# Kernel optimization log

Measured on AMD Instinct MI355X. Metric: run time of the kernel, lower is better.

Reference implementation:

```python
import jax, jax.numpy as jnp
import numpy as np

L, H, M, KB = 8, 512, 32, 256  # layers, hidden, fourier modes, key bits
EPS = 1e-5


def setup_inputs() -> dict:
    key = jax.random.key(0)
    ks = jax.random.split(key, 20)
    B, S = 8, 2048
    s = 0.02
    return {
        'x': jax.random.normal(ks[0], (B, S), jnp.float32),
        # input projection Linear(1, H): weight [H] (squeezed), bias [H]
        'in_w': jax.random.normal(ks[1], (H,), jnp.float32) * s,
        'in_b': jax.random.normal(ks[2], (H,), jnp.float32) * s,
        # per-layer fourier weights (complex, stored as real/imag), conv1d(k=1), layernorm
        'fw_r': jax.random.normal(ks[3], (L, M, H, H), jnp.float32) * s,
        'fw_i': jax.random.normal(ks[4], (L, M, H, H), jnp.float32) * s,
        'conv_w': jax.random.normal(ks[5], (L, H, H), jnp.float32) / np.sqrt(H),
        'conv_b': jax.random.normal(ks[6], (L, H), jnp.float32) * s,
        'ln_g': jnp.ones((L, H), jnp.float32),
        'ln_b': jnp.zeros((L, H), jnp.float32),
        # output projection H -> H/2 -> H/4 -> 1
        'op1_w': jax.random.normal(ks[7], (H // 2, H), jnp.float32) / np.sqrt(H),
        'op1_b': jnp.zeros((H // 2,), jnp.float32),
        'op2_w': jax.random.normal(ks[8], (H // 4, H // 2), jnp.float32) / np.sqrt(H // 2),
        'op2_b': jnp.zeros((H // 4,), jnp.float32),
        'op3_w': jax.random.normal(ks[9], (1, H // 4), jnp.float32) / np.sqrt(H // 4),
        'op3_b': jnp.zeros((1,), jnp.float32),
        # cryptanalytic head H -> H -> KB (sigmoid)
        'h1_w': jax.random.normal(ks[10], (H, H), jnp.float32) / np.sqrt(H),
        'h1_b': jnp.zeros((H,), jnp.float32),
        'h2_w': jax.random.normal(ks[11], (KB, H), jnp.float32) / np.sqrt(H),
        'h2_b': jnp.zeros((KB,), jnp.float32),
    }


def _gelu(x):
    return jax.nn.gelu(x, approximate=False)


def _fourier_layer(x, Wc, cw, cb, g, b):
    # x: [B, S, H]; Wc: [M, H, H] complex
    S = x.shape[1]
    x_ft = jnp.fft.rfft(x, axis=1)  # [B, F, H] complex, F = S//2+1
    m = min(M, x_ft.shape[1])
    # batched per-mode complex GEMM (replaces python loop over modes)
    spec = jnp.einsum('bmh,mhk->bmk', x_ft[:, :m], Wc[:m])
    out_ft = jnp.concatenate([spec, jnp.zeros_like(x_ft[:, m:])], axis=1)
    x_fourier = jnp.fft.irfft(out_ft, n=S, axis=1)  # real [B, S, H]
    x_conv = x @ cw.T + cb  # Conv1d kernel-size-1 == per-position linear
    y = x_fourier + x_conv
    mu = jnp.mean(y, axis=-1, keepdims=True)
    var = jnp.var(y, axis=-1, keepdims=True)
    return (y - mu) * jax.lax.rsqrt(var + EPS) * g + b


def reference(x, in_w, in_b, fw_r, fw_i, conv_w, conv_b, ln_g, ln_b,
              op1_w, op1_b, op2_w, op2_b, op3_w, op3_b,
              h1_w, h1_b, h2_w, h2_b):
    # input projection: Linear(1, H) on x[..., None]
    h = x[:, :, None] * in_w[None, None, :] + in_b  # [B, S, H]
    Wc = fw_r + 1j * fw_i  # [L, M, H, H]
    for l in range(L):
        h = _fourier_layer(h, Wc[l], conv_w[l], conv_b[l], ln_g[l], ln_b[l]) + h
    # output projection (dropout is identity in eval)
    o = _gelu(h @ op1_w.T + op1_b)
    o = _gelu(o @ op2_w.T + op2_b)
    output = (o @ op3_w.T + op3_b)[..., 0]  # [B, S]
    gf = jnp.mean(h, axis=1)  # [B, H]
    k = _gelu(gf @ h1_w.T + h1_b)
    key_pred = jax.nn.sigmoid(k @ h2_w.T + h2_b)  # [B, KB]
    return output, key_pred
```

## Files before the change

kernel.cpp:

```cpp
#include <hip/hip_runtime.h>
#include <hip/hip_bf16.h>
#include <math.h>

#define BB   8
#define SEQ  2048
#define HD   512
#define LAY  8
#define MD   32
#define NKB  256
#define LNEPS 1e-5f

typedef __attribute__((ext_vector_type(8))) short v8s;
typedef __attribute__((ext_vector_type(4))) float v4f;
typedef __attribute__((ext_vector_type(4))) unsigned short v4us;

__device__ __forceinline__ float b2f(__hip_bfloat16 v) { return __bfloat162float(v); }
__device__ __forceinline__ float geluf(float v) { return v * 0.5f * (1.f + erff(v * 0.70710678118654752f)); }
__device__ __forceinline__ float bflo(unsigned int u) { return __uint_as_float((u & 0xFFFFu) << 16); }
__device__ __forceinline__ float bfhi(unsigned int u) { return __uint_as_float(u & 0xFFFF0000u); }

__device__ __forceinline__ float ldin(const void* p, size_t i, int bf) {
    if (bf) return __bfloat162float(((const __hip_bfloat16*)p)[i]);
    return ((const float*)p)[i];
}
__device__ __forceinline__ void stout(void* p, size_t i, float v, int bf) {
    if (bf) ((__hip_bfloat16*)p)[i] = __float2bfloat16(v);
    else    ((float*)p)[i] = v;
}

__device__ __forceinline__ void gl2lds16(const void* g, void* l) {
    __builtin_amdgcn_global_load_lds((__attribute__((address_space(1))) void*)g,
                                     (__attribute__((address_space(3))) void*)l, 16, 0, 0);
}

__global__ void k_flag(const unsigned int* __restrict__ lng_bits, int* __restrict__ flag) {
    if (threadIdx.x == 0 && blockIdx.x == 0)
        *flag = (lng_bits[0] == 0x3F803F80u) ? 1 : 0;
}

__global__ void k_setup(const void* __restrict__ x, const void* __restrict__ in_w, const void* __restrict__ in_b,
                        const void* __restrict__ cw, const void* __restrict__ w1, const void* __restrict__ w2,
                        const void* __restrict__ h1w, const void* __restrict__ h2w,
                        __hip_bfloat16* __restrict__ Ffwd, __hip_bfloat16* __restrict__ T2,
                        __hip_bfloat16* __restrict__ cwbf, __hip_bfloat16* __restrict__ w1bf,
                        __hip_bfloat16* __restrict__ w2bf, float* __restrict__ h1T, float* __restrict__ h2T,
                        float* __restrict__ h, __hip_bfloat16* __restrict__ hbf,
                        float* __restrict__ gf,
                        const int* __restrict__ flag) {
    int bf = *flag;
    int blk = blockIdx.x, t = threadIdx.x;
    if (blk < 512) {
        int idx = blk * 256 + t;
        int j = idx >> 11, s = idx & 2047;
        int m = j >> 1;
        int phase = (m * s) & (SEQ - 1);
        float ang = (float)phase * (6.283185307179586f / (float)SEQ);
        Ffwd[idx] = __float2bfloat16((j & 1) ? -sinf(ang) : cosf(ang));
    } else if (blk < 1024) {
        int idx = (blk - 512) * 256 + t;
        int s = idx >> 6, j = idx & 63;
        int m = j >> 1;
        float v;
        if (j == 0)      v = 1.f / (float)SEQ;
        else if (j == 1) v = 0.f;
        else {
            int phase = (m * s) & (SEQ - 1);
            float ang = (float)phase * (6.283185307179586f / (float)SEQ);
            v = (j & 1) ? (-2.f / (float)SEQ) * sinf(ang) : (2.f / (float)SEQ) * cosf(ang);
        }
        T2[idx] = __float2bfloat16(v);
    } else if (blk < 9216) {
        int idx = (blk - 1024) * 256 + t;
        cwbf[idx] = __float2bfloat16(ldin(cw, idx, bf));
    } else if (blk < 9728) {
        int idx = (blk - 9216) * 256 + t;
        w1bf[idx] = __float2bfloat16(ldin(w1, idx, bf));
    } else if (blk < 9856) {
        int idx = (blk - 9728) * 256 + t;
        w2bf[idx] = __float2bfloat16(ldin(w2, idx, bf));
    } else if (blk < 10880) {
        int idx = (blk - 9856) * 256 + t;
        int r = idx & 511, c = idx >> 9;
        h1T[idx] = ldin(h1w, (size_t)r * 512 + c, bf);
    } else if (blk < 11392) {
        int idx = (blk - 10880) * 256 + t;
        int r = idx & 255, c = idx >> 8;
        h2T[idx] = ldin(h2w, (size_t)r * 512 + c, bf);
    } else if (blk < 11408) {
        int idx = (blk - 11392) * 256 + t;
        gf[idx] = 0.f;
    } else {
        int idx = (blk - 11408) * 256 + t;
        int j = idx & 511;
        int bs = idx >> 9;
        float v = ldin(x, bs, bf) * ldin(in_w, j, bf) + ldin(in_b, j, bf);
        h[idx] = v;
        hbf[idx] = __float2bfloat16(v);
    }
}

__global__ __launch_bounds__(256) void k_fdft2(const __hip_bfloat16* __restrict__ hbf,
                                               const __hip_bfloat16* __restrict__ Ffwd,
                                               float* __restrict__ Xpart) {
    __shared__ __align__(16) __hip_bfloat16 Als[2][16 * 72];
    int t = threadIdx.x;
    int lane = t & 63, wv = t >> 6;
    int ln15 = lane & 15, quad = lane >> 4;
    int ht = blockIdx.x, b = blockIdx.y, kh = blockIdx.z;
    int kcs = kh * 16;
    int sr = t >> 2, hc = (t & 3) * 4;

    v4f acc = (v4f){0.f, 0.f, 0.f, 0.f};

    const __hip_bfloat16* asrc0 = hbf + (size_t)b * SEQ * HD + ht * 16;
    const __hip_bfloat16* fbase = Ffwd + (size_t)(wv * 16 + ln15) * SEQ + quad * 8;

    v4us cur = *(const v4us*)(asrc0 + (size_t)(kcs * 64 + sr) * HD + hc);
#pragma unroll
    for (int e = 0; e < 4; e++)
        Als[0][(hc + e) * 72 + sr] = ((const __hip_bfloat16*)&cur)[e];
    __syncthreads();
    for (int i = 0; i < 16; i++) {
        int buf = i & 1;
        v4us nxt = cur;
        if (i < 15)
            nxt = *(const v4us*)(asrc0 + (size_t)((kcs + i + 1) * 64 + sr) * HD + hc);
        v8s bf0 = *(const v8s*)(fbase + (kcs + i) * 64);
        v8s bf1 = *(const v8s*)(fbase + (kcs + i) * 64 + 32);
        v8s af0 = *(const v8s*)&Als[buf][ln15 * 72 + quad * 8];
        v8s af1 = *(const v8s*)&Als[buf][ln15 * 72 + 32 + quad * 8];
        acc = __builtin_amdgcn_mfma_f32_16x16x32_bf16(af0, bf0, acc, 0, 0, 0);
        acc = __builtin_amdgcn_mfma_f32_16x16x32_bf16(af1, bf1, acc, 0, 0, 0);
        if (i < 15) {
#pragma unroll
            for (int e = 0; e < 4; e++)
                Als[buf ^ 1][(hc + e) * 72 + sr] = ((const __hip_bfloat16*)&nxt)[e];
        }
        __syncthreads();
        cur = nxt;
    }
    int j = wv * 16 + ln15;
    int m = j >> 1, c = j & 1;
    int hg = ht * 16 + quad * 4;
    float* outp = Xpart + (size_t)kh * 262144 + (size_t)(b * 32 + m) * 1024;
#pragma unroll
    for (int r = 0; r < 4; r++)
        outp[(size_t)(hg + r) * 2 + c] = acc[r];
}

__global__ __launch_bounds__(512) void k_mix(const float* __restrict__ Xp0, const float* __restrict__ Xp1,
                                             const void* __restrict__ fwr, const void* __restrict__ fwi,
                                             __hip_bfloat16* __restrict__ spec2, int l,
                                             const int* __restrict__ flag) {
    int bf = *flag;
    int kt = blockIdx.x;
    int m  = blockIdx.y;
    int t = threadIdx.x;
    int kl = t & 15, hg = t >> 4;
    int k0 = kt * 64 + kl * 4;
    __shared__ float xs[8192];
    __shared__ float red[32 * 512];
    for (int e = t; e < 8192; e += 512) {
        int bb = e >> 10, r = e & 1023;
        size_t off = (size_t)(bb * 32 + m) * 1024 + r;
        xs[bb * 1024 + r] = Xp0[off] + Xp1[off];
    }
    __syncthreads();
    float ar[8][4], ai[8][4];
#pragma unroll
    for (int bb = 0; bb < 8; bb++)
#pragma unroll
        for (int q = 0; q < 4; q++) { ar[bb][q] = 0.f; ai[bb][q] = 0.f; }
    size_t wbase = (size_t)(l * 32 + m) * 262144 + k0;
    const float2* xs2 = (const float2*)xs;
    if (bf) {
        const __hip_bfloat16* fr = (const __hip_bfloat16*)fwr;
        const __hip_bfloat16* fi = (const __hip_bfloat16*)fwi;
#pragma unroll 2
        for (int hh = hg; hh < 512; hh += 32) {
            v4us urv = *(const v4us*)(fr + wbase + (size_t)hh * 512);
            v4us uiv = *(const v4us*)(fi + wbase + (size_t)hh * 512);
            float wr[4], wi[4];
#pragma unroll
            for (int q = 0; q < 4; q++) {
                wr[q] = __uint_as_float(((unsigned int)(unsigned short)urv[q]) << 16);
                wi[q] = __uint_as_float(((unsigned int)(unsigned short)uiv[q]) << 16);
            }
#pragma unroll
            for (int bb = 0; bb < 8; bb++) {
                float2 x2 = xs2[bb * 512 + hh];
#pragma unroll
                for (int q = 0; q < 4; q++) {
                    ar[bb][q] += x2.x * wr[q] - x2.y * wi[q];
                    ai[bb][q] += x2.x * wi[q] + x2.y * wr[q];
                }
            }
        }
    } else {
        const float* fr = (const float*)fwr;
        const float* fi = (const float*)fwi;
#pragma unroll 2
        for (int hh = hg; hh < 512; hh += 32) {
            v4f wrv = *(const v4f*)(fr + wbase + (size_t)hh * 512);
            v4f wiv = *(const v4f*)(fi + wbase + (size_t)hh * 512);
#pragma unroll
            for (int bb = 0; bb < 8; bb++) {
                float2 x2 = xs2[bb * 512 + hh];
#pragma unroll
                for (int q = 0; q < 4; q++) {
                    ar[bb][q] += x2.x * wrv[q] - x2.y * wiv[q];
                    ai[bb][q] += x2.x * wiv[q] + x2.y * wrv[q];
                }
            }
        }
    }
    v4f* red4 = (v4f*)red;
#pragma unroll
    for (int bb = 0; bb < 8; bb++)
        red4[hg * 128 + bb * 16 + kl] = (v4f){ar[bb][0], ar[bb][1], ar[bb][2], ar[bb][3]};
    __syncthreads();
    float sr = 0.f;
#pragma unroll
    for (int g = 0; g < 32; g++) sr += red[g * 512 + t];
    __syncthreads();
#pragma unroll
    for (int bb = 0; bb < 8; bb++)
        red4[hg * 128 + bb * 16 + kl] = (v4f){ai[bb][0], ai[bb][1], ai[bb][2], ai[bb][3]};
    __syncthreads();
    float si = 0.f;
#pragma unroll
    for (int g = 0; g < 32; g++) si += red[g * 512 + t];

    int bb = t >> 6, j = t & 63;
    int k = kt * 64 + j;
    size_t o = ((size_t)(bb * 512 + k) << 6) + 2 * m;
    __hip_bfloat16 hr = __float2bfloat16(sr), hi = __float2bfloat16(si);
    unsigned int pk = (unsigned int)*(unsigned short*)&hr | ((unsigned int)*(unsigned short*)&hi << 16);
    *(unsigned int*)(spec2 + o) = pk;
}

__global__ __launch_bounds__(512) void k_gln(__hip_bfloat16* __restrict__ hbf,
                                             const __hip_bfloat16* __restrict__ cwbf,
                                             const __hip_bfloat16* __restrict__ T2,
                                             const __hip_bfloat16* __restrict__ spec2,
                                             const void* __restrict__ cb,
                                             const void* __restrict__ lng, const void* __restrict__ lnb,
                                             float* __restrict__ h,
                                             int l, const int* __restrict__ flag) {
    int bfv = *flag;
    __shared__ __align__(16) __hip_bfloat16 smem[2][18432];
    __shared__ float stats[128];
    __hip_bfloat16* Yls = &smem[0][0];

    int t = threadIdx.x;
    int lane = t & 63, wv = t >> 6;
    int wr = wv >> 2, wc = wv & 3;
    int ln15 = lane & 15, quad = lane >> 4;
    int row0 = blockIdx.x * 64;
    int b = row0 >> 11, s0 = row0 & 2047;

    v4f acc[16];
#pragma unroll
    for (int i = 0; i < 16; i++) acc[i] = (v4f){0.f, 0.f, 0.f, 0.f};

    const __hip_bfloat16* cwl = cwbf + (size_t)l * 262144;

    auto stage = [&](int buf, int kc) {
        int k0 = kc * 32;
        if (t < 256) {
            int row = t >> 2, kq = (t & 3) * 8;
            const __hip_bfloat16* asrc = (k0 < 512)
                ? hbf + (size_t)(row0 + row) * 512 + k0 + kq
                : T2 + (size_t)(s0 + row) * 64 + (k0 - 512) + kq;
            gl2lds16(asrc, &smem[buf][(size_t)(wv * 64) * 8]);
        }
#pragma unroll
        for (int p = 0; p < 4; p++) {
            int i = p * 512 + t;
            int n = i >> 2, kq = (i & 3) * 8;
            const __hip_bfloat16* bsrc = (k0 < 512)
                ? cwl + (size_t)n * 512 + k0 + kq
                : spec2 + (size_t)(b * 512 + n) * 64 + (k0 - 512) + kq;
            gl2lds16(bsrc, &smem[buf][2048 + (size_t)(p * 512 + wv * 64) * 8]);
        }
    };

    stage(0, 0);
    __syncthreads();
    int cur = 0;
    for (int kc = 0; kc < 18; kc++) {
        if (kc < 17) stage(cur ^ 1, kc + 1);
        const __hip_bfloat16* Als = &smem[cur][0];
        const __hip_bfloat16* Bls = &smem[cur][2048];
        v8s af[2], bfr[8];
#pragma unroll
        for (int i = 0; i < 2; i++)
            af[i] = *(const v8s*)&Als[(wr * 32 + i * 16 + ln15) * 32 + quad * 8];
#pragma unroll
        for (int j = 0; j < 8; j++)
            bfr[j] = *(const v8s*)&Bls[(wc * 128 + j * 16 + ln15) * 32 + quad * 8];
#pragma unroll
        for (int i = 0; i < 2; i++)
#pragma unroll
            for (int j = 0; j < 8; j++)
                acc[i * 8 + j] = __builtin_amdgcn_mfma_f32_16x16x32_bf16(af[i], bfr[j], acc[i * 8 + j], 0, 0, 0);
        __syncthreads();
        cur ^= 1;
    }
#pragma unroll
    for (int j = 0; j < 8; j++) {
        int col = wc * 128 + j * 16 + ln15;
        float cbv = ldin(cb, l * HD + col, bfv);
#pragma unroll
        for (int i = 0; i < 2; i++) {
            int rl = wr * 32 + i * 16 + quad * 4;
#pragma unroll
            for (int r = 0; r < 4; r++)
                Yls[(rl + r) * 520 + col] = __float2bfloat16(acc[i * 8 + j][r] + cbv);
        }
    }
    __syncthreads();
    {
        int r = t >> 3, g = t & 7;
        float s = 0.f, q = 0.f;
        for (int i = 0; i < 32; i++) {
            int cp = g + i * 8;
            unsigned int u = *(const unsigned int*)&Yls[r * 520 + cp * 2];
            float v0 = bflo(u), v1 = bfhi(u);
            s += v0 + v1; q += v0 * v0 + v1 * v1;
        }
        s += __shfl_xor(s, 1); s += __shfl_xor(s, 2); s += __shfl_xor(s, 4);
        q += __shfl_xor(q, 1); q += __shfl_xor(q, 2); q += __shfl_xor(q, 4);
        if (g == 0) {
            float mu = s * (1.f / (float)HD);
            float var = q * (1.f / (float)HD) - mu * mu;
            stats[r * 2] = mu; stats[r * 2 + 1] = rsqrtf(var + LNEPS);
        }
    }
    __syncthreads();
    {
        int c2 = t & 255;
        int gc = 2 * c2;
        float g0 = ldin(lng, l * HD + gc, bfv),     g1 = ldin(lng, l * HD + gc + 1, bfv);
        float b0 = ldin(lnb, l * HD + gc, bfv),     b1 = ldin(lnb, l * HD + gc + 1, bfv);
        int rbase = t >> 8;
        for (int k = 0; k < 32; k++) {
            int r = rbase + 2 * k;
            float mu = stats[r * 2], rs = stats[r * 2 + 1];
            unsigned int u = *(const unsigned int*)&Yls[r * 520 + c2 * 2];
            float v0 = bflo(u), v1 = bfhi(u);
            float2 hv = *(const float2*)&h[(size_t)(row0 + r) * HD + gc];
            float n0 = (v0 - mu) * rs * g0 + b0 + hv.x;
            float n1 = (v1 - mu) * rs * g1 + b1 + hv.y;
            *(float2*)&h[(size_t)(row0 + r) * HD + gc] = (float2){n0, n1};
            __hip_bfloat16 a0 = __float2bfloat16(n0), a1 = __float2bfloat16(n1);
            unsigned int up = ((unsigned int)(*(unsigned short*)&a1) << 16) | (unsigned int)(*(unsigned short*)&a0);
            ((unsigned int*)(hbf + (size_t)(row0 + r) * HD))[c2] = up;
        }
    }
}

__global__ __launch_bounds__(256) void k_pj1(const __hip_bfloat16* __restrict__ hbf,
                                             const __hip_bfloat16* __restrict__ w1bf,
                                             const void* __restrict__ b1,
                                             __hip_bfloat16* __restrict__ o1bf,
                                             const int* __restrict__ flag) {
    int bfv = *flag;
    __shared__ __align__(16) __hip_bfloat16 smem[2][8192];
    int t = threadIdx.x;
    int lane = t & 63, wv = t >> 6;
    int wr = wv >> 1, wc = wv & 1;
    int ln15 = lane & 15, quad = lane >> 4;
    int row0 = blockIdx.x * 128, n0 = blockIdx.y * 128;

    v4f acc[16];
#pragma unroll
    for (int i = 0; i < 16; i++) acc[i] = (v4f){0.f, 0.f, 0.f, 0.f};

    auto stage = [&](int buf, int kc) {
        int k0 = kc * 32;
#pragma unroll
        for (int p = 0; p < 2; p++) {
            int i = p * 256 + t;
            int row = i >> 2, kq = (i & 3) * 8;
            gl2lds16(hbf + (size_t)(row0 + row) * 512 + k0 + kq, &smem[buf][(size_t)(p * 256 + wv * 64) * 8]);
            gl2lds16(w1bf + (size_t)(n0 + row) * 512 + k0 + kq, &smem[buf][4096 + (size_t)(p * 256 + wv * 64) * 8]);
        }
    };

    stage(0, 0);
    __syncthreads();
    int cur = 0;
    for (int kc = 0; kc < 16; kc++) {
        if (kc < 15) stage(cur ^ 1, kc + 1);
        const __hip_bfloat16* Als = &smem[cur][0];
        const __hip_bfloat16* Bls = &smem[cur][4096];
        v8s af[4], bfr[4];
#pragma unroll
        for (int i = 0; i < 4; i++)
            af[i] = *(const v8s*)&Als[(wr * 64 + i * 16 + ln15) * 32 + quad * 8];
#pragma unroll
        for (int j = 0; j < 4; j++)
            bfr[j] = *(const v8s*)&Bls[(wc * 64 + j * 16 + ln15) * 32 + quad * 8];
#pragma unroll
        for (int i = 0; i < 4; i++)
#pragma unroll
            for (int j = 0; j < 4; j++)
                acc[i * 4 + j] = __builtin_amdgcn_mfma_f32_16x16x32_bf16(af[i], bfr[j], acc[i * 4 + j], 0, 0, 0);
        __syncthreads();
        cur ^= 1;
    }
#pragma unroll
    for (int j = 0; j < 4; j++) {
        int col = n0 + wc * 64 + j * 16 + ln15;
        float bv = ldin(b1, col, bfv);
#pragma unroll
        for (int i = 0; i < 4; i++) {
            int rg = row0 + wr * 64 + i * 16 + quad * 4;
#pragma unroll
            for (int r = 0; r < 4; r++)
                o1bf[(size_t)(rg + r) * 256 + col] = __float2bfloat16(geluf(acc[i * 4 + j][r] + bv));
        }
    }
}

__global__ __launch_bounds__(256) void k_pj2(const __hip_bfloat16* __restrict__ o1bf,
                                             const __hip_bfloat16* __restrict__ w2bf,
                                             const void* __restrict__ b2,
                                             const void* __restrict__ w3, const void* __restrict__ b3,
                                             void* __restrict__ out, const int* __restrict__ flag) {
    int bfv = *flag;
    __shared__ __align__(16) __hip_bfloat16 smem[2][8192];
    __shared__ __hip_bfloat16 o2s[128 * 130];
    __shared__ float w3s[128];
    int t = threadIdx.x;
    int lane = t & 63, wv = t >> 6;
    int wr = wv >> 1, wc = wv & 1;
    int ln15 = lane & 15, quad = lane >> 4;
    int row0 = blockIdx.x * 128;
    if (t < 128) w3s[t] = ldin(w3, t, bfv);

    v4f acc[16];
#pragma unroll
    for (int i = 0; i < 16; i++) acc[i] = (v4f){0.f, 0.f, 0.f, 0.f};

    auto stage = [&](int buf, int kc) {
        int k0 = kc * 32;
#pragma unroll
        for (int p = 0; p < 2; p++) {
            int i = p * 256 + t;
            int row = i >> 2, kq = (i & 3) * 8;
            gl2lds16(o1bf + (size_t)(row0 + row) * 256 + k0 + kq, &smem[buf][(size_t)(p * 256 + wv * 64) * 8]);
            gl2lds16(w2bf + (size_t)row * 256 + k0 + kq,          &smem[buf][4096 + (size_t)(p * 256 + wv * 64) * 8]);
        }
    };

    stage(0, 0);
    __syncthreads();
    int cur = 0;
    for (int kc = 0; kc < 8; kc++) {
        if (kc < 7) stage(cur ^ 1, kc + 1);
        const __hip_bfloat16* Als = &smem[cur][0];
        const __hip_bfloat16* Bls = &smem[cur][4096];
        v8s af[4], bfr[4];
#pragma unroll
        for (int i = 0; i < 4; i++)
            af[i] = *(const v8s*)&Als[(wr * 64 + i * 16 + ln15) * 32 + quad * 8];
#pragma unroll
        for (int j = 0; j < 4; j++)
            bfr[j] = *(const v8s*)&Bls[(wc * 64 + j * 16 + ln15) * 32 + quad * 8];
#pragma unroll
        for (int i = 0; i < 4; i++)
#pragma unroll
            for (int j = 0; j < 4; j++)
                acc[i * 4 + j] = __builtin_amdgcn_mfma_f32_16x16x32_bf16(af[i], bfr[j], acc[i * 4 + j], 0, 0, 0);
        __syncthreads();
        cur ^= 1;
    }
#pragma unroll
    for (int j = 0; j < 4; j++) {
        int col = wc * 64 + j * 16 + ln15;
        float bv = ldin(b2, col, bfv);
#pragma unroll
        for (int i = 0; i < 4; i++) {
            int rl = wr * 64 + i * 16 + quad * 4;
#pragma unroll
            for (int r = 0; r < 4; r++)
                o2s[(rl + r) * 130 + col] = __float2bfloat16(geluf(acc[i * 4 + j][r] + bv));
        }
    }
    __syncthreads();
    if (t < 128) {
        float s = 0.f;
        for (int j = 0; j < 128; j++) s += b2f(o2s[t * 130 + j]) * w3s[j];
        stout(out, row0 + t, s + ldin(b3, 0, bfv), bfv);
    }
}

__global__ __launch_bounds__(512) void k_gf(const float* __restrict__ h, float* __restrict__ gf) {
    int sc = blockIdx.x, b = blockIdx.y;
    int j = threadIdx.x;
    const float* p = h + ((size_t)b * SEQ + sc * 64) * HD + j;
    float s = 0.f;
    for (int i = 0; i < 64; i++) s += p[(size_t)i * HD];
    atomicAdd(&gf[b * HD + j], s * (1.f / (float)SEQ));
}

__global__ __launch_bounds__(512) void k_head(const float* __restrict__ gf,
                                              const float* __restrict__ h1T, const void* __restrict__ h1b,
                                              const float* __restrict__ h2T, const void* __restrict__ h2b,
                                              void* __restrict__ out, const int* __restrict__ flag) {
    int bf = *flag;
    int b = blockIdx.x;
    int t = threadIdx.x;
    __shared__ float gs[512];
    __shared__ float ks[512];
    gs[t] = gf[b * HD + t];
    __syncthreads();
    float a = 0.f;
    for (int j = 0; j < 512; j++) a += gs[j] * h1T[j * 512 + t];
    ks[t] = geluf(a + ldin(h1b, t, bf));
    __syncthreads();
    if (t < 256) {
        float s = 0.f;
        for (int j = 0; j < 512; j++) s += ks[j] * h2T[j * 256 + t];
        s += ldin(h2b, t, bf);
        stout(out, BB * SEQ + b * NKB + t, 1.f / (1.f + expf(-s)), bf);
    }
}

extern "C" void kernel_launch(void* const* d_in, const int* in_sizes, int n_in,
                              void* d_out, int out_size, void* d_ws, size_t ws_size,
                              hipStream_t stream) {
    const void* x    = d_in[0];
    const void* in_w = d_in[1];
    const void* in_b = d_in[2];
    const void* fwr  = d_in[3];
    const void* fwi  = d_in[4];
    const void* cw   = d_in[5];
    const void* cb   = d_in[6];
    const void* lng  = d_in[7];
    const void* lnb  = d_in[8];
    const void* w1   = d_in[9];
    const void* b1   = d_in[10];
    const void* w2   = d_in[11];
    const void* b2   = d_in[12];
    const void* w3   = d_in[13];
    const void* b3   = d_in[14];
    const void* h1w  = d_in[15];
    const void* h1b  = d_in[16];
    const void* h2w  = d_in[17];
    const void* h2b  = d_in[18];

    float* ws = (float*)d_ws;
    __hip_bfloat16* Ffwd = (__hip_bfloat16*)ws;
    float*          h    = ws + 131072;
    float*          Xp   = h + 8388608;
    __hip_bfloat16* o1bf = (__hip_bfloat16*)Xp;
    __hip_bfloat16* hbf  = (__hip_bfloat16*)(Xp + 4194304);
    __hip_bfloat16* cwbf = (__hip_bfloat16*)(Xp + 8388608);
    __hip_bfloat16* T2   = (__hip_bfloat16*)(Xp + 10485760);
    __hip_bfloat16* spec2= (__hip_bfloat16*)(Xp + 10551296);
    float*          XftOld = Xp + 10682368;
    float*          gf   = XftOld + 262144;
    float*          w1T  = gf + 4096;
    __hip_bfloat16* w1bf = (__hip_bfloat16*)w1T;
    __hip_bfloat16* w2bf = (__hip_bfloat16*)(w1T + 65536);
    float*          w2T  = w1T + 131072;
    float*          h1T  = w2T + 32768;
    float*          h2T  = h1T + 262144;
    int*            flag = (int*)(h2T + 131072);
    float*          Xpart = h2T + 131072 + 64;

    k_flag<<<1, 1, 0, stream>>>((const unsigned int*)lng, flag);
    k_setup<<<44176, 256, 0, stream>>>(x, in_w, in_b, cw, w1, w2, h1w, h2w,
                                       Ffwd, T2, cwbf, w1bf, w2bf, h1T, h2T,
                                       h, hbf, gf, flag);

    for (int l = 0; l < LAY; l++) {
        k_fdft2<<<dim3(32, 8, 2), 256, 0, stream>>>(hbf, Ffwd, Xpart);
        k_mix<<<dim3(8, 32), 512, 0, stream>>>(Xpart, Xpart + 262144, fwr, fwi, spec2, l, flag);
        k_gln<<<256, 512, 0, stream>>>(hbf, cwbf, T2, spec2, cb, lng, lnb, h, l, flag);
    }

    k_gf<<<dim3(32, 8), 512, 0, stream>>>(h, gf);
    k_pj1<<<dim3(128, 2), 256, 0, stream>>>(hbf, w1bf, b1, o1bf, flag);
    k_pj2<<<128, 256, 0, stream>>>(o1bf, w2bf, b2, w3, b3, d_out, flag);
    k_head<<<8, 512, 0, stream>>>(gf, h1T, h1b, h2T, h2b, d_out, flag);
}
```

Baseline: 1.189 ms.

## Fuse per-layer DFT, mode-mix and GEMM+LayerNorm into one persistent kernel

Replaces the 24 per-layer launches (forward DFT, spectral mixing, conv GEMM plus LayerNorm) with a single persistent 256-block kernel. The stages are separated by a software grid barrier built on global atomics, and shared memory is reused across stages. This removes launch overhead and inter-kernel gaps. In exchange it relies on all 256 blocks being co-resident, adds spin-wait barrier costs, and locks each stage to the same block and thread geometry.

```diff
diff --git a/kernel.cpp b/kernel.cpp
--- a/kernel.cpp
+++ b/kernel.cpp
@@ -33,6 +33,22 @@
                                      (__attribute__((address_space(3))) void*)l, 16, 0, 0);
 }
 
+__device__ void gbar(int* bar, int t) {
+    __syncthreads();
+    if (t == 0) {
+        int g = __hip_atomic_load(&bar[1], __ATOMIC_RELAXED, __HIP_MEMORY_SCOPE_AGENT);
+        int v = __hip_atomic_fetch_add(&bar[0], 1, __ATOMIC_ACQ_REL, __HIP_MEMORY_SCOPE_AGENT);
+        if (v == 255) {
+            __hip_atomic_store(&bar[0], 0, __ATOMIC_RELAXED, __HIP_MEMORY_SCOPE_AGENT);
+            __hip_atomic_store(&bar[1], g + 1, __ATOMIC_RELEASE, __HIP_MEMORY_SCOPE_AGENT);
+        } else {
+            while (__hip_atomic_load(&bar[1], __ATOMIC_ACQUIRE, __HIP_MEMORY_SCOPE_AGENT) == g)
+                __builtin_amdgcn_s_sleep(2);
+        }
+    }
+    __syncthreads();
+}
+
 __global__ void k_flag(const unsigned int* __restrict__ lng_bits, int* __restrict__ flag) {
     if (threadIdx.x == 0 && blockIdx.x == 0)
         *flag = (lng_bits[0] == 0x3F803F80u) ? 1 : 0;
@@ -45,7 +61,7 @@
                         __hip_bfloat16* __restrict__ cwbf, __hip_bfloat16* __restrict__ w1bf,
                         __hip_bfloat16* __restrict__ w2bf, float* __restrict__ h1T, float* __restrict__ h2T,
                         float* __restrict__ h, __hip_bfloat16* __restrict__ hbf,
-                        float* __restrict__ gf,
+                        float* __restrict__ gf, int* __restrict__ bar,
                         const int* __restrict__ flag) {
     int bf = *flag;
     int blk = blockIdx.x, t = threadIdx.x;
@@ -89,6 +105,7 @@
     } else if (blk < 11408) {
         int idx = (blk - 11392) * 256 + t;
         gf[idx] = 0.f;
+        if (blk == 11392 && t < 4) bar[t] = 0;
     } else {
         int idx = (blk - 11408) * 256 + t;
         int j = idx & 511;
@@ -99,264 +116,269 @@
     }
 }
 
-__global__ __launch_bounds__(256) void k_fdft2(const __hip_bfloat16* __restrict__ hbf,
-                                               const __hip_bfloat16* __restrict__ Ffwd,
-                                               float* __restrict__ Xpart) {
-    __shared__ __align__(16) __hip_bfloat16 Als[2][16 * 72];
-    int t = threadIdx.x;
-    int lane = t & 63, wv = t >> 6;
-    int ln15 = lane & 15, quad = lane >> 4;
-    int ht = blockIdx.x, b = blockIdx.y, kh = blockIdx.z;
-    int kcs = kh * 16;
-    int sr = t >> 2, hc = (t & 3) * 4;
-
-    v4f acc = (v4f){0.f, 0.f, 0.f, 0.f};
-
-    const __hip_bfloat16* asrc0 = hbf + (size_t)b * SEQ * HD + ht * 16;
-    const __hip_bfloat16* fbase = Ffwd + (size_t)(wv * 16 + ln15) * SEQ + quad * 8;
-
-    v4us cur = *(const v4us*)(asrc0 + (size_t)(kcs * 64 + sr) * HD + hc);
-#pragma unroll
-    for (int e = 0; e < 4; e++)
-        Als[0][(hc + e) * 72 + sr] = ((const __hip_bfloat16*)&cur)[e];
-    __syncthreads();
-    for (int i = 0; i < 16; i++) {
-        int buf = i & 1;
-        v4us nxt = cur;
-        if (i < 15)
-            nxt = *(const v4us*)(asrc0 + (size_t)((kcs + i + 1) * 64 + sr) * HD + hc);
-        v8s bf0 = *(const v8s*)(fbase + (kcs + i) * 64);
-        v8s bf1 = *(const v8s*)(fbase + (kcs + i) * 64 + 32);
-        v8s af0 = *(const v8s*)&Als[buf][ln15 * 72 + quad * 8];
-        v8s af1 = *(const v8s*)&Als[buf][ln15 * 72 + 32 + quad * 8];
-        acc = __builtin_amdgcn_mfma_f32_16x16x32_bf16(af0, bf0, acc, 0, 0, 0);
-        acc = __builtin_amdgcn_mfma_f32_16x16x32_bf16(af1, bf1, acc, 0, 0, 0);
-        if (i < 15) {
+__global__ __launch_bounds__(512, 1) void k_layers(
+        __hip_bfloat16* __restrict__ hbf, const __hip_bfloat16* __restrict__ Ffwd,
+        float* __restrict__ Xpart,
+        const void* __restrict__ fwr, const void* __restrict__ fwi,
+        __hip_bfloat16* __restrict__ spec2,
+        const __hip_bfloat16* __restrict__ cwbf, const __hip_bfloat16* __restrict__ T2,
+        const void* __restrict__ cb, const void* __restrict__ lng, const void* __restrict__ lnb,
+        float* __restrict__ h, int* __restrict__ bar, const int* __restrict__ flag) {
+    __shared__ __align__(16) char smem[98304];
+    __shared__ float stats[128];
+    int t = threadIdx.x, bid = blockIdx.x;
+    int bfv = *flag;
+
+    for (int l = 0; l < LAY; l++) {
+        {
+            int unit = t >> 8, tt = t & 255;
+            int g = bid * 2 + unit;
+            int ht = g & 31, b = (g >> 5) & 7, kh = g >> 8;
+            int lane = tt & 63, wv = tt >> 6;
+            int ln15 = lane & 15, quad = lane >> 4;
+            int kcs = kh * 16;
+            int sr = tt >> 2, hc = (tt & 3) * 4;
+
+            v4f acc = (v4f){0.f, 0.f, 0.f, 0.f};
+            const __hip_bfloat16* asrc0 = hbf + (size_t)b * SEQ * HD + ht * 16;
+            const __hip_bfloat16* fbase = Ffwd + (size_t)(wv * 16 + ln15) * SEQ + quad * 8;
+            __hip_bfloat16* A0 = (__hip_bfloat16*)smem + unit * 2304;
+
+            v4us cur = *(const v4us*)(asrc0 + (size_t)(kcs * 64 + sr) * HD + hc);
 #pragma unroll
             for (int e = 0; e < 4; e++)
-                Als[buf ^ 1][(hc + e) * 72 + sr] = ((const __hip_bfloat16*)&nxt)[e];
-        }
-        __syncthreads();
-        cur = nxt;
-    }
-    int j = wv * 16 + ln15;
-    int m = j >> 1, c = j & 1;
-    int hg = ht * 16 + quad * 4;
-    float* outp = Xpart + (size_t)kh * 262144 + (size_t)(b * 32 + m) * 1024;
-#pragma unroll
-    for (int r = 0; r < 4; r++)
-        outp[(size_t)(hg + r) * 2 + c] = acc[r];
-}
-
-__global__ __launch_bounds__(512) void k_mix(const float* __restrict__ Xp0, const float* __restrict__ Xp1,
-                                             const void* __restrict__ fwr, const void* __restrict__ fwi,
-                                             __hip_bfloat16* __restrict__ spec2, int l,
-                                             const int* __restrict__ flag) {
-    int bf = *flag;
-    int kt = blockIdx.x;
-    int m  = blockIdx.y;
-    int t = threadIdx.x;
-    int kl = t & 15, hg = t >> 4;
-    int k0 = kt * 64 + kl * 4;
-    __shared__ float xs[8192];
-    __shared__ float red[32 * 512];
-    for (int e = t; e < 8192; e += 512) {
-        int bb = e >> 10, r = e & 1023;
-        size_t off = (size_t)(bb * 32 + m) * 1024 + r;
-        xs[bb * 1024 + r] = Xp0[off] + Xp1[off];
-    }
-    __syncthreads();
-    float ar[8][4], ai[8][4];
-#pragma unroll
-    for (int bb = 0; bb < 8; bb++)
-#pragma unroll
-        for (int q = 0; q < 4; q++) { ar[bb][q] = 0.f; ai[bb][q] = 0.f; }
-    size_t wbase = (size_t)(l * 32 + m) * 262144 + k0;
-    const float2* xs2 = (const float2*)xs;
-    if (bf) {
-        const __hip_bfloat16* fr = (const __hip_bfloat16*)fwr;
-        const __hip_bfloat16* fi = (const __hip_bfloat16*)fwi;
+                A0[(hc + e) * 72 + sr] = ((const __hip_bfloat16*)&cur)[e];
+            __syncthreads();
+            for (int i = 0; i < 16; i++) {
+                int buf = i & 1;
+                v4us nxt = cur;
+                if (i < 15)
+                    nxt = *(const v4us*)(asrc0 + (size_t)((kcs + i + 1) * 64 + sr) * HD + hc);
+                v8s bf0 = *(const v8s*)(fbase + (kcs + i) * 64);
+                v8s bf1 = *(const v8s*)(fbase + (kcs + i) * 64 + 32);
+                const __hip_bfloat16* Ab = A0 + buf * 1152;
+                v8s af0 = *(const v8s*)&Ab[ln15 * 72 + quad * 8];
+                v8s af1 = *(const v8s*)&Ab[ln15 * 72 + 32 + quad * 8];
+                acc = __builtin_amdgcn_mfma_f32_16x16x32_bf16(af0, bf0, acc, 0, 0, 0);
+                acc = __builtin_amdgcn_mfma_f32_16x16x32_bf16(af1, bf1, acc, 0, 0, 0);
+                if (i < 15) {
+                    __hip_bfloat16* An = A0 + (buf ^ 1) * 1152;
+#pragma unroll
+                    for (int e = 0; e < 4; e++)
+                        An[(hc + e) * 72 + sr] = ((const __hip_bfloat16*)&nxt)[e];
+                }
+                __syncthreads();
+                cur = nxt;
+            }
+            int j = wv * 16 + ln15;
+            int m = j >> 1, c = j & 1;
+            int hg = ht * 16 + quad * 4;
+            float* outp = Xpart + (size_t)kh * 262144 + (size_t)(b * 32 + m) * 1024;
+#pragma unroll
+            for (int r = 0; r < 4; r++)
+                outp[(size_t)(hg + r) * 2 + c] = acc[r];
+        }
+        gbar(bar, t);
+        {
+            int kt = bid & 7;
+            int m  = bid >> 3;
+            int kl = t & 15, hg = t >> 4;
+            int k0 = kt * 64 + kl * 4;
+            float* xs  = (float*)smem;
+            float* red = (float*)(smem + 32768);
+            const float* Xp0 = Xpart;
+            const float* Xp1 = Xpart + 262144;
+            for (int e = t; e < 8192; e += 512) {
+                int bb = e >> 10, r = e & 1023;
+                size_t off = (size_t)(bb * 32 + m) * 1024 + r;
+                xs[bb * 1024 + r] = Xp0[off] + Xp1[off];
+            }
+            __syncthreads();
+            float ar[8][4], ai[8][4];
+#pragma unroll
+            for (int bb = 0; bb < 8; bb++)
+#pragma unroll
+                for (int q = 0; q < 4; q++) { ar[bb][q] = 0.f; ai[bb][q] = 0.f; }
+            size_t wbase = (size_t)(l * 32 + m) * 262144 + k0;
+            const float2* xs2 = (const float2*)xs;
+            if (bfv) {
+                const __hip_bfloat16* fr = (const __hip_bfloat16*)fwr;
+                const __hip_bfloat16* fi = (const __hip_bfloat16*)fwi;
 #pragma unroll 2
-        for (int hh = hg; hh < 512; hh += 32) {
-            v4us urv = *(const v4us*)(fr + wbase + (size_t)hh * 512);
-            v4us uiv = *(const v4us*)(fi + wbase + (size_t)hh * 512);
-            float wr[4], wi[4];
-#pragma unroll
-            for (int q = 0; q < 4; q++) {
-                wr[q] = __uint_as_float(((unsigned int)(unsigned short)urv[q]) << 16);
-                wi[q] = __uint_as_float(((unsigned int)(unsigned short)uiv[q]) << 16);
+                for (int hh = hg; hh < 512; hh += 32) {
+                    v4us urv = *(const v4us*)(fr + wbase + (size_t)hh * 512);
+                    v4us uiv = *(const v4us*)(fi + wbase + (size_t)hh * 512);
+                    float wr[4], wi[4];
+#pragma unroll
+                    for (int q = 0; q < 4; q++) {
+                        wr[q] = __uint_as_float(((unsigned int)(unsigned short)urv[q]) << 16);
+                        wi[q] = __uint_as_float(((unsigned int)(unsigned short)uiv[q]) << 16);
+                    }
+#pragma unroll
+                    for (int bb = 0; bb < 8; bb++) {
+                        float2 x2 = xs2[bb * 512 + hh];
+#pragma unroll
+                        for (int q = 0; q < 4; q++) {
+                            ar[bb][q] += x2.x * wr[q] - x2.y * wi[q];
+                            ai[bb][q] += x2.x * wi[q] + x2.y * wr[q];
+                        }
+                    }
+                }
+            } else {
+                const float* fr = (const float*)fwr;
+                const float* fi = (const float*)fwi;
+#pragma unroll 2
+                for (int hh = hg; hh < 512; hh += 32) {
+                    v4f wrv = *(const v4f*)(fr + wbase + (size_t)hh * 512);
+                    v4f wiv = *(const v4f*)(fi + wbase + (size_t)hh * 512);
+#pragma unroll
+                    for (int bb = 0; bb < 8; bb++) {
+                        float2 x2 = xs2[bb * 512 + hh];
+#pragma unroll
+                        for (int q = 0; q < 4; q++) {
+                            ar[bb][q] += x2.x * wrv[q] - x2.y * wiv[q];
+                            ai[bb][q] += x2.x * wiv[q] + x2.y * wrv[q];
+                        }
+                    }
+                }
             }
-#pragma unroll
-            for (int bb = 0; bb < 8; bb++) {
-                float2 x2 = xs2[bb * 512 + hh];
-#pragma unroll
-                for (int q = 0; q < 4; q++) {
-                    ar[bb][q] += x2.x * wr[q] - x2.y * wi[q];
-                    ai[bb][q] += x2.x * wi[q] + x2.y * wr[q];
-                }
+            v4f* red4 = (v4f*)red;
+#pragma unroll
+            for (int bb = 0; bb < 8; bb++)
+                red4[hg * 128 + bb * 16 + kl] = (v4f){ar[bb][0], ar[bb][1], ar[bb][2], ar[bb][3]};
+            __syncthreads();
+            float sr = 0.f;
+#pragma unroll
+            for (int g2 = 0; g2 < 32; g2++) sr += red[g2 * 512 + t];
+            __syncthreads();
+#pragma unroll
+            for (int bb = 0; bb < 8; bb++)
+                red4[hg * 128 + bb * 16 + kl] = (v4f){ai[bb][0], ai[bb][1], ai[bb][2], ai[bb][3]};
+            __syncthreads();
+            float si = 0.f;
+#pragma unroll
+            for (int g2 = 0; g2 < 32; g2++) si += red[g2 * 512 + t];
+
+            int bb = t >> 6, j = t & 63;
+            int k = kt * 64 + j;
+            size_t o = ((size_t)(bb * 512 + k) << 6) + 2 * m;
+            __hip_bfloat16 hr = __float2bfloat16(sr), hi = __float2bfloat16(si);
+            unsigned int pk = (unsigned int)*(unsigned short*)&hr | ((unsigned int)*(unsigned short*)&hi << 16);
+            *(unsigned int*)(spec2 + o) = pk;
+        }
+        gbar(bar, t);
+        {
+            __hip_bfloat16* SM0 = (__hip_bfloat16*)smem;
+            __hip_bfloat16* SM1 = (__hip_bfloat16*)smem + 18432;
+            __hip_bfloat16* Yls = (__hip_bfloat16*)smem;
+
+            int lane = t & 63, wv = t >> 6;
+            int wr = wv >> 2, wc = wv & 3;
+            int ln15 = lane & 15, quad = lane >> 4;
+            int row0 = bid * 64;
+            int b = row0 >> 11, s0 = row0 & 2047;
+
+            v4f acc[16];
+#pragma unroll
+            for (int i = 0; i < 16; i++) acc[i] = (v4f){0.f, 0.f, 0.f, 0.f};
+
+            const __hip_bfloat16* cwl = cwbf + (size_t)l * 262144;
+
+            auto stage = [&](__hip_bfloat16* dst, int kc) {
+                int k0 = kc * 32;
+                if (t < 256) {
+                    int row = t >> 2, kq = (t & 3) * 8;
+                    const __hip_bfloat16* asrc = (k0 < 512)
+                        ? hbf + (size_t)(row0 + row) * 512 + k0 + kq
+                        : T2 + (size_t)(s0 + row) * 64 + (k0 - 512) + kq;
+                    gl2lds16(asrc, dst + (size_t)(wv * 64) * 8);
+                }
+#pragma unroll
+                for (int p = 0; p < 4; p++) {
+                    int i = p * 512 + t;
+                    int n = i >> 2, kq = (i & 3) * 8;
+                    const __hip_bfloat16* bsrc = (k0 < 512)
+                        ? cwl + (size_t)n * 512 + k0 + kq
+                        : spec2 + (size_t)(b * 512 + n) * 64 + (k0 - 512) + kq;
+                    gl2lds16(bsrc, dst + 2048 + (size_t)(p * 512 + wv * 64) * 8);
+                }
+            };
+
+            stage(SM0, 0);
+            __syncthreads();
+            int cur = 0;
+            for (int kc = 0; kc < 18; kc++) {
+                if (kc < 17) stage(cur ? SM0 : SM1, kc + 1);
+                const __hip_bfloat16* Als = cur ? SM1 : SM0;
+                const __hip_bfloat16* Bls = Als + 2048;
+                v8s af[2], bfr[8];
+#pragma unroll
+                for (int i = 0; i < 2; i++)
+                    af[i] = *(const v8s*)&Als[(wr * 32 + i * 16 + ln15) * 32 + quad * 8];
+#pragma unroll
+                for (int j = 0; j < 8; j++)
+                    bfr[j] = *(const v8s*)&Bls[(wc * 128 + j * 16 + ln15) * 32 + quad * 8];
+#pragma unroll
+                for (int i = 0; i < 2; i++)
+#pragma unroll
+                    for (int j = 0; j < 8; j++)
+                        acc[i * 8 + j] = __builtin_amdgcn_mfma_f32_16x16x32_bf16(af[i], bfr[j], acc[i * 8 + j], 0, 0, 0);
+                __syncthreads();
+                cur ^= 1;
             }
-        }
-    } else {
-        const float* fr = (const float*)fwr;
-        const float* fi = (const float*)fwi;
-#pragma unroll 2
-        for (int hh = hg; hh < 512; hh += 32) {
-            v4f wrv = *(const v4f*)(fr + wbase + (size_t)hh * 512);
-            v4f wiv = *(const v4f*)(fi + wbase + (size_t)hh * 512);
-#pragma unroll
-            for (int bb = 0; bb < 8; bb++) {
-                float2 x2 = xs2[bb * 512 + hh];
-#pragma unroll
-                for (int q = 0; q < 4; q++) {
-                    ar[bb][q] += x2.x * wrv[q] - x2.y * wiv[q];
-                    ai[bb][q] += x2.x * wiv[q] + x2.y * wrv[q];
+#pragma unroll
+            for (int j = 0; j < 8; j++) {
+                int col = wc * 128 + j * 16 + ln15;
+                float cbv = ldin(cb, l * HD + col, bfv);
+#pragma unroll
+                for (int i = 0; i < 2; i++) {
+                    int rl = wr * 32 + i * 16 + quad * 4;
+#pragma unroll
+                    for (int r = 0; r < 4; r++)
+                        Yls[(rl + r) * 520 + col] = __float2bfloat16(acc[i * 8 + j][r] + cbv);
                 }
             }
-        }
-    }
-    v4f* red4 = (v4f*)red;
-#pragma unroll
-    for (int bb = 0; bb < 8; bb++)
-        red4[hg * 128 + bb * 16 + kl] = (v4f){ar[bb][0], ar[bb][1], ar[bb][2], ar[bb][3]};
-    __syncthreads();
-    float sr = 0.f;
-#pragma unroll
-    for (int g = 0; g < 32; g++) sr += red[g * 512 + t];
-    __syncthreads();
-#pragma unroll
-    for (int bb = 0; bb < 8; bb++)
-        red4[hg * 128 + bb * 16 + kl] = (v4f){ai[bb][0], ai[bb][1], ai[bb][2], ai[bb][3]};
-    __syncthreads();
-    float si = 0.f;
-#pragma unroll
-    for (int g = 0; g < 32; g++) si += red[g * 512 + t];
-
-    int bb = t >> 6, j = t & 63;
-    int k = kt * 64 + j;
-    size_t o = ((size_t)(bb * 512 + k) << 6) + 2 * m;
-    __hip_bfloat16 hr = __float2bfloat16(sr), hi = __float2bfloat16(si);
-    unsigned int pk = (unsigned int)*(unsigned short*)&hr | ((unsigned int)*(unsigned short*)&hi << 16);
-    *(unsigned int*)(spec2 + o) = pk;
-}
-
-__global__ __launch_bounds__(512) void k_gln(__hip_bfloat16* __restrict__ hbf,
-                                             const __hip_bfloat16* __restrict__ cwbf,
-                                             const __hip_bfloat16* __restrict__ T2,
-                                             const __hip_bfloat16* __restrict__ spec2,
-                                             const void* __restrict__ cb,
-                                             const void* __restrict__ lng, const void* __restrict__ lnb,
-                                             float* __restrict__ h,
-                                             int l, const int* __restrict__ flag) {
-    int bfv = *flag;
-    __shared__ __align__(16) __hip_bfloat16 smem[2][18432];
-    __shared__ float stats[128];
-    __hip_bfloat16* Yls = &smem[0][0];
-
-    int t = threadIdx.x;
-    int lane = t & 63, wv = t >> 6;
-    int wr = wv >> 2, wc = wv & 3;
-    int ln15 = lane & 15, quad = lane >> 4;
-    int row0 = blockIdx.x * 64;
-    int b = row0 >> 11, s0 = row0 & 2047;
-
-    v4f acc[16];
-#pragma unroll
-    for (int i = 0; i < 16; i++) acc[i] = (v4f){0.f, 0.f, 0.f, 0.f};
-
-    const __hip_bfloat16* cwl = cwbf + (size_t)l * 262144;
-
-    auto stage = [&](int buf, int kc) {
-        int k0 = kc * 32;
-        if (t < 256) {
-            int row = t >> 2, kq = (t & 3) * 8;
-            const __hip_bfloat16* asrc = (k0 < 512)
-                ? hbf + (size_t)(row0 + row) * 512 + k0 + kq
-                : T2 + (size_t)(s0 + row) * 64 + (k0 - 512) + kq;
-            gl2lds16(asrc, &smem[buf][(size_t)(wv * 64) * 8]);
-        }
-#pragma unroll
-        for (int p = 0; p < 4; p++) {
-            int i = p * 512 + t;
-            int n = i >> 2, kq = (i & 3) * 8;
-            const __hip_bfloat16* bsrc = (k0 < 512)
-                ? cwl + (size_t)n * 512 + k0 + kq
-                : spec2 + (size_t)(b * 512 + n) * 64 + (k0 - 512) + kq;
-            gl2lds16(bsrc, &smem[buf][2048 + (size_t)(p * 512 + wv * 64) * 8]);
-        }
-    };
-
-    stage(0, 0);
-    __syncthreads();
-    int cur = 0;
-    for (int kc = 0; kc < 18; kc++) {
-        if (kc < 17) stage(cur ^ 1, kc + 1);
-        const __hip_bfloat16* Als = &smem[cur][0];
-        const __hip_bfloat16* Bls = &smem[cur][2048];
-        v8s af[2], bfr[8];
-#pragma unroll
-        for (int i = 0; i < 2; i++)
-            af[i] = *(const v8s*)&Als[(wr * 32 + i * 16 + ln15) * 32 + quad * 8];
-#pragma unroll
-        for (int j = 0; j < 8; j++)
-            bfr[j] = *(const v8s*)&Bls[(wc * 128 + j * 16 + ln15) * 32 + quad * 8];
-#pragma unroll
-        for (int i = 0; i < 2; i++)
-#pragma unroll
-            for (int j = 0; j < 8; j++)
-                acc[i * 8 + j] = __builtin_amdgcn_mfma_f32_16x16x32_bf16(af[i], bfr[j], acc[i * 8 + j], 0, 0, 0);
-        __syncthreads();
-        cur ^= 1;
-    }
-#pragma unroll
-    for (int j = 0; j < 8; j++) {
-        int col = wc * 128 + j * 16 + ln15;
-        float cbv = ldin(cb, l * HD + col, bfv);
-#pragma unroll
-        for (int i = 0; i < 2; i++) {
-            int rl = wr * 32 + i * 16 + quad * 4;
-#pragma unroll
-            for (int r = 0; r < 4; r++)
-                Yls[(rl + r) * 520 + col] = __float2bfloat16(acc[i * 8 + j][r] + cbv);
-        }
-    }
-    __syncthreads();
-    {
-        int r = t >> 3, g = t & 7;
-        float s = 0.f, q = 0.f;
-        for (int i = 0; i < 32; i++) {
-            int cp = g + i * 8;
-            unsigned int u = *(const unsigned int*)&Yls[r * 520 + cp * 2];
-            float v0 = bflo(u), v1 = bfhi(u);
-            s += v0 + v1; q += v0 * v0 + v1 * v1;
-        }
-        s += __shfl_xor(s, 1); s += __shfl_xor(s, 2); s += __shfl_xor(s, 4);
-        q += __shfl_xor(q, 1); q += __shfl_xor(q, 2); q += __shfl_xor(q, 4);
-        if (g == 0) {
-            float mu = s * (1.f / (float)HD);
-            float var = q * (1.f / (float)HD) - mu * mu;
-            stats[r * 2] = mu; stats[r * 2 + 1] = rsqrtf(var + LNEPS);
-        }
-    }
-    __syncthreads();
-    {
-        int c2 = t & 255;
-        int gc = 2 * c2;
-        float g0 = ldin(lng, l * HD + gc, bfv),     g1 = ldin(lng, l * HD + gc + 1, bfv);
-        float b0 = ldin(lnb, l * HD + gc, bfv),     b1 = ldin(lnb, l * HD + gc + 1, bfv);
-        int rbase = t >> 8;
-        for (int k = 0; k < 32; k++) {
-            int r = rbase + 2 * k;
-            float mu = stats[r * 2], rs = stats[r * 2 + 1];
-            unsigned int u = *(const unsigned int*)&Yls[r * 520 + c2 * 2];
-            float v0 = bflo(u), v1 = bfhi(u);
-            float2 hv = *(const float2*)&h[(size_t)(row0 + r) * HD + gc];
-            float n0 = (v0 - mu) * rs * g0 + b0 + hv.x;
-            float n1 = (v1 - mu) * rs * g1 + b1 + hv.y;
-            *(float2*)&h[(size_t)(row0 + r) * HD + gc] = (float2){n0, n1};
-            __hip_bfloat16 a0 = __float2bfloat16(n0), a1 = __float2bfloat16(n1);
-            unsigned int up = ((unsigned int)(*(unsigned short*)&a1) << 16) | (unsigned int)(*(unsigned short*)&a0);
-            ((unsigned int*)(hbf + (size_t)(row0 + r) * HD))[c2] = up;
-        }
+            __syncthreads();
+            {
+                int r = t >> 3, g2 = t & 7;
+                float s = 0.f, q = 0.f;
+                for (int i = 0; i < 32; i++) {
+                    int cp = g2 + i * 8;
+                    unsigned int u = *(const unsigned int*)&Yls[r * 520 + cp * 2];
+                    float v0 = bflo(u), v1 = bfhi(u);
+                    s += v0 + v1; q += v0 * v0 + v1 * v1;
+                }
+                s += __shfl_xor(s, 1); s += __shfl_xor(s, 2); s += __shfl_xor(s, 4);
+                q += __shfl_xor(q, 1); q += __shfl_xor(q, 2); q += __shfl_xor(q, 4);
+                if (g2 == 0) {
+                    float mu = s * (1.f / (float)HD);
+                    float var = q * (1.f / (float)HD) - mu * mu;
+                    stats[r * 2] = mu; stats[r * 2 + 1] = rsqrtf(var + LNEPS);
+                }
+            }
+            __syncthreads();
+            {
+                int c2 = t & 255;
+                int gc = 2 * c2;
+                float g0 = ldin(lng, l * HD + gc, bfv),     g1 = ldin(lng, l * HD + gc + 1, bfv);
+                float b0 = ldin(lnb, l * HD + gc, bfv),     b1 = ldin(lnb, l * HD + gc + 1, bfv);
+                int rbase = t >> 8;
+                for (int k = 0; k < 32; k++) {
+                    int r = rbase + 2 * k;
+                    float mu = stats[r * 2], rs = stats[r * 2 + 1];
+                    unsigned int u = *(const unsigned int*)&Yls[r * 520 + c2 * 2];
+                    float v0 = bflo(u), v1 = bfhi(u);
+                    float2 hv = *(const float2*)&h[(size_t)(row0 + r) * HD + gc];
+                    float n0 = (v0 - mu) * rs * g0 + b0 + hv.x;
+                    float n1 = (v1 - mu) * rs * g1 + b1 + hv.y;
+                    *(float2*)&h[(size_t)(row0 + r) * HD + gc] = (float2){n0, n1};
+                    __hip_bfloat16 a0 = __float2bfloat16(n0), a1 = __float2bfloat16(n1);
+                    unsigned int up = ((unsigned int)(*(unsigned short*)&a1) << 16) | (unsigned int)(*(unsigned short*)&a0);
+                    ((unsigned int*)(hbf + (size_t)(row0 + r) * HD))[c2] = up;
+                }
+            }
+        }
+        if (l < LAY - 1) gbar(bar, t);
     }
 }
 
@@ -571,17 +593,15 @@
     float*          h2T  = h1T + 262144;
     int*            flag = (int*)(h2T + 131072);
     float*          Xpart = h2T + 131072 + 64;
+    int*            bar  = (int*)(Xpart + 524288);
 
     k_flag<<<1, 1, 0, stream>>>((const unsigned int*)lng, flag);
     k_setup<<<44176, 256, 0, stream>>>(x, in_w, in_b, cw, w1, w2, h1w, h2w,
                                        Ffwd, T2, cwbf, w1bf, w2bf, h1T, h2T,
-                                       h, hbf, gf, flag);
-
-    for (int l = 0; l < LAY; l++) {
-        k_fdft2<<<dim3(32, 8, 2), 256, 0, stream>>>(hbf, Ffwd, Xpart);
-        k_mix<<<dim3(8, 32), 512, 0, stream>>>(Xpart, Xpart + 262144, fwr, fwi, spec2, l, flag);
-        k_gln<<<256, 512, 0, stream>>>(hbf, cwbf, T2, spec2, cb, lng, lnb, h, l, flag);
-    }
+                                       h, hbf, gf, bar, flag);
+
+    k_layers<<<256, 512, 0, stream>>>(hbf, Ffwd, Xpart, fwr, fwi, spec2,
+                                      cwbf, T2, cb, lng, lnb, h, bar, flag);
 
     k_gf<<<dim3(32, 8), 512, 0, stream>>>(h, gf);
     k_pj1<<<dim3(128, 2), 256, 0, stream>>>(hbf, w1bf, b1, o1bf, flag);
```

Measured after the change: 1.994 ms. 1.68x slower.

## Raise split-K in forward DFT and retile spectral mix with shuffle reduction

Applied to the files above, without the earlier changes.

The forward DFT kernel now splits the sequence reduction four ways instead of two, doubling its block count. The spectral-mix kernel sums the four partials and uses 32-wide output-column tiles, doubling its grid. It reduces over the hidden dimension first with warp shuffles, which cuts its large shared-memory reduction buffer to a small one. The aim is more parallelism and occupancy in these latency- and bandwidth-bound per-layer kernels, at the cost of extra partial-sum traffic and a larger Xpart scratch area that must fit in the workspace.

```diff
diff --git a/kernel.cpp b/kernel.cpp
--- a/kernel.cpp
+++ b/kernel.cpp
@@ -107,7 +107,7 @@
     int lane = t & 63, wv = t >> 6;
     int ln15 = lane & 15, quad = lane >> 4;
     int ht = blockIdx.x, b = blockIdx.y, kh = blockIdx.z;
-    int kcs = kh * 16;
+    int kcs = kh * 8;
     int sr = t >> 2, hc = (t & 3) * 4;
 
     v4f acc = (v4f){0.f, 0.f, 0.f, 0.f};
@@ -120,10 +120,10 @@
     for (int e = 0; e < 4; e++)
         Als[0][(hc + e) * 72 + sr] = ((const __hip_bfloat16*)&cur)[e];
     __syncthreads();
-    for (int i = 0; i < 16; i++) {
+    for (int i = 0; i < 8; i++) {
         int buf = i & 1;
         v4us nxt = cur;
-        if (i < 15)
+        if (i < 7)
             nxt = *(const v4us*)(asrc0 + (size_t)((kcs + i + 1) * 64 + sr) * HD + hc);
         v8s bf0 = *(const v8s*)(fbase + (kcs + i) * 64);
         v8s bf1 = *(const v8s*)(fbase + (kcs + i) * 64 + 32);
@@ -131,7 +131,7 @@
         v8s af1 = *(const v8s*)&Als[buf][ln15 * 72 + 32 + quad * 8];
         acc = __builtin_amdgcn_mfma_f32_16x16x32_bf16(af0, bf0, acc, 0, 0, 0);
         acc = __builtin_amdgcn_mfma_f32_16x16x32_bf16(af1, bf1, acc, 0, 0, 0);
-        if (i < 15) {
+        if (i < 7) {
 #pragma unroll
             for (int e = 0; e < 4; e++)
                 Als[buf ^ 1][(hc + e) * 72 + sr] = ((const __hip_bfloat16*)&nxt)[e];
@@ -148,7 +148,7 @@
         outp[(size_t)(hg + r) * 2 + c] = acc[r];
 }
 
-__global__ __launch_bounds__(512) void k_mix(const float* __restrict__ Xp0, const float* __restrict__ Xp1,
+__global__ __launch_bounds__(512) void k_mix(const float* __restrict__ Xpart,
                                              const void* __restrict__ fwr, const void* __restrict__ fwi,
                                              __hip_bfloat16* __restrict__ spec2, int l,
                                              const int* __restrict__ flag) {
@@ -156,14 +156,14 @@
     int kt = blockIdx.x;
     int m  = blockIdx.y;
     int t = threadIdx.x;
-    int kl = t & 15, hg = t >> 4;
-    int k0 = kt * 64 + kl * 4;
+    int kl = t & 7, hg = t >> 3;
+    int k0 = kt * 32 + kl * 4;
     __shared__ float xs[8192];
-    __shared__ float red[32 * 512];
+    __shared__ float red[8 * 256];
     for (int e = t; e < 8192; e += 512) {
         int bb = e >> 10, r = e & 1023;
         size_t off = (size_t)(bb * 32 + m) * 1024 + r;
-        xs[bb * 1024 + r] = Xp0[off] + Xp1[off];
+        xs[bb * 1024 + r] = Xpart[off] + Xpart[off + 262144] + Xpart[off + 524288] + Xpart[off + 786432];
     }
     __syncthreads();
     float ar[8][4], ai[8][4];
@@ -176,8 +176,8 @@
     if (bf) {
         const __hip_bfloat16* fr = (const __hip_bfloat16*)fwr;
         const __hip_bfloat16* fi = (const __hip_bfloat16*)fwi;
-#pragma unroll 2
-        for (int hh = hg; hh < 512; hh += 32) {
+#pragma unroll 4
+        for (int hh = hg; hh < 512; hh += 64) {
             v4us urv = *(const v4us*)(fr + wbase + (size_t)hh * 512);
             v4us uiv = *(const v4us*)(fi + wbase + (size_t)hh * 512);
             float wr[4], wi[4];
@@ -199,8 +199,8 @@
     } else {
         const float* fr = (const float*)fwr;
         const float* fi = (const float*)fwi;
-#pragma unroll 2
-        for (int hh = hg; hh < 512; hh += 32) {
+#pragma unroll 4
+        for (int hh = hg; hh < 512; hh += 64) {
             v4f wrv = *(const v4f*)(fr + wbase + (size_t)hh * 512);
             v4f wiv = *(const v4f*)(fi + wbase + (size_t)hh * 512);
 #pragma unroll
@@ -214,29 +214,48 @@
             }
         }
     }
-    v4f* red4 = (v4f*)red;
 #pragma unroll
     for (int bb = 0; bb < 8; bb++)
-        red4[hg * 128 + bb * 16 + kl] = (v4f){ar[bb][0], ar[bb][1], ar[bb][2], ar[bb][3]};
-    __syncthreads();
-    float sr = 0.f;
-#pragma unroll
-    for (int g = 0; g < 32; g++) sr += red[g * 512 + t];
-    __syncthreads();
-#pragma unroll
-    for (int bb = 0; bb < 8; bb++)
-        red4[hg * 128 + bb * 16 + kl] = (v4f){ai[bb][0], ai[bb][1], ai[bb][2], ai[bb][3]};
-    __syncthreads();
-    float si = 0.f;
-#pragma unroll
-    for (int g = 0; g < 32; g++) si += red[g * 512 + t];
-
-    int bb = t >> 6, j = t & 63;
-    int k = kt * 64 + j;
-    size_t o = ((size_t)(bb * 512 + k) << 6) + 2 * m;
-    __hip_bfloat16 hr = __float2bfloat16(sr), hi = __float2bfloat16(si);
-    unsigned int pk = (unsigned int)*(unsigned short*)&hr | ((unsigned int)*(unsigned short*)&hi << 16);
-    *(unsigned int*)(spec2 + o) = pk;
+#pragma unroll
+        for (int q = 0; q < 4; q++) {
+            float vr = ar[bb][q], vi = ai[bb][q];
+            vr += __shfl_xor(vr, 8);  vr += __shfl_xor(vr, 16); vr += __shfl_xor(vr, 32);
+            vi += __shfl_xor(vi, 8);  vi += __shfl_xor(vi, 16); vi += __shfl_xor(vi, 32);
+            ar[bb][q] = vr; ai[bb][q] = vi;
+        }
+    int w = t >> 6, lane = t & 63;
+    float sr = 0.f, si = 0.f;
+    if (lane < 8) {
+#pragma unroll
+        for (int bb = 0; bb < 8; bb++)
+#pragma unroll
+            for (int q = 0; q < 4; q++)
+                red[w * 256 + bb * 32 + kl * 4 + q] = ar[bb][q];
+    }
+    __syncthreads();
+    if (t < 256) {
+#pragma unroll
+        for (int g = 0; g < 8; g++) sr += red[g * 256 + t];
+    }
+    __syncthreads();
+    if (lane < 8) {
+#pragma unroll
+        for (int bb = 0; bb < 8; bb++)
+#pragma unroll
+            for (int q = 0; q < 4; q++)
+                red[w * 256 + bb * 32 + kl * 4 + q] = ai[bb][q];
+    }
+    __syncthreads();
+    if (t < 256) {
+#pragma unroll
+        for (int g = 0; g < 8; g++) si += red[g * 256 + t];
+        int b = t >> 5, kloc = t & 31;
+        int k = kt * 32 + kloc;
+        size_t o = ((size_t)(b * 512 + k) << 6) + 2 * m;
+        __hip_bfloat16 hr = __float2bfloat16(sr), hi = __float2bfloat16(si);
+        unsigned int pk = (unsigned int)*(unsigned short*)&hr | ((unsigned int)*(unsigned short*)&hi << 16);
+        *(unsigned int*)(spec2 + o) = pk;
+    }
 }
 
 __global__ __launch_bounds__(512) void k_gln(__hip_bfloat16* __restrict__ hbf,
@@ -321,17 +340,17 @@
     }
     __syncthreads();
     {
-        int r = t >> 3, g = t & 7;
+        int r = t >> 3, g2 = t & 7;
         float s = 0.f, q = 0.f;
         for (int i = 0; i < 32; i++) {
-            int cp = g + i * 8;
+            int cp = g2 + i * 8;
             unsigned int u = *(const unsigned int*)&Yls[r * 520 + cp * 2];
             float v0 = bflo(u), v1 = bfhi(u);
             s += v0 + v1; q += v0 * v0 + v1 * v1;
         }
         s += __shfl_xor(s, 1); s += __shfl_xor(s, 2); s += __shfl_xor(s, 4);
         q += __shfl_xor(q, 1); q += __shfl_xor(q, 2); q += __shfl_xor(q, 4);
-        if (g == 0) {
+        if (g2 == 0) {
             float mu = s * (1.f / (float)HD);
             float var = q * (1.f / (float)HD) - mu * mu;
             stats[r * 2] = mu; stats[r * 2 + 1] = rsqrtf(var + LNEPS);
@@ -578,8 +597,8 @@
                                        h, hbf, gf, flag);
 
     for (int l = 0; l < LAY; l++) {
-        k_fdft2<<<dim3(32, 8, 2), 256, 0, stream>>>(hbf, Ffwd, Xpart);
-        k_mix<<<dim3(8, 32), 512, 0, stream>>>(Xpart, Xpart + 262144, fwr, fwi, spec2, l, flag);
+        k_fdft2<<<dim3(32, 8, 4), 256, 0, stream>>>(hbf, Ffwd, Xpart);
+        k_mix<<<dim3(16, 32), 512, 0, stream>>>(Xpart, fwr, fwi, spec2, l, flag);
         k_gln<<<256, 512, 0, stream>>>(hbf, cwbf, T2, spec2, cb, lng, lnb, h, l, flag);
     }
 
```

Measured after the change: 1.231 ms. 3.5% more time.
